# Optimization experiments

Hardware: AMD Instinct MI355X
Metric: run time of the kernel (lower is better)

Reference implementation:

```python
import jax, jax.numpy as jnp
import numpy as np

N_NODES = 1_000_000
N_EDGES = 2_000_000
N_GRAPHS = 50_000
X_DIM = 5
E_DIM = 1
HIDDEN = 110  # num_kernel1_Nhop+..+num_kernel4_Nhop = 10+20+30+50
G_DIM = 5    # graph_embedding_dim
BN_EPS = 1e-5


def setup_inputs() -> dict:
    key = jax.random.key(0)
    ks = jax.random.split(key, 12)
    inp = {
        "x": jax.random.normal(ks[0], (N_NODES, X_DIM), jnp.float32),
        "edge_attr": jax.random.normal(ks[1], (N_EDGES, E_DIM), jnp.float32),
        "batch": jnp.sort(jax.random.randint(ks[2], (N_NODES,), 0, N_GRAPHS)),
        "edge_index": jax.random.randint(ks[3], (2, N_EDGES), 0, N_NODES),
        # BatchNorm affine params
        "bn_x_gamma": jnp.ones((X_DIM,), jnp.float32),
        "bn_x_beta": jnp.zeros((X_DIM,), jnp.float32),
        "bn_e_gamma": jnp.ones((E_DIM,), jnp.float32),
        "bn_e_beta": jnp.zeros((E_DIM,), jnp.float32),
        # stand-in MolGCN params (node transform + edge message mix)
        "W_gnn": jax.random.normal(ks[4], (X_DIM, HIDDEN), jnp.float32) / np.sqrt(X_DIM),
        "b_gnn": jnp.zeros((HIDDEN,), jnp.float32),
        "W_e": jax.random.normal(ks[5], (E_DIM, HIDDEN), jnp.float32),
        # readout head: graph_embedding_lin1 / lin2
        "W1": jax.random.normal(ks[6], (HIDDEN, G_DIM), jnp.float32) / np.sqrt(HIDDEN),
        "b1": jnp.zeros((G_DIM,), jnp.float32),
        "W2": jax.random.normal(ks[7], (G_DIM, G_DIM), jnp.float32) / np.sqrt(G_DIM),
        "b2": jnp.zeros((G_DIM,), jnp.float32),
    }
    return inp


def _batch_norm(v, gamma, beta):
    # train-mode BatchNorm1d math: biased batch statistics
    mu = v.mean(axis=0)
    var = ((v - mu) ** 2).mean(axis=0)
    return (v - mu) * jax.lax.rsqrt(var + BN_EPS) * gamma + beta


def reference(x, edge_attr, batch, edge_index,
              bn_x_gamma, bn_x_beta, bn_e_gamma, bn_e_beta,
              W_gnn, b_gnn, W_e, W1, b1, W2, b2):
    # node / edge batch norms
    xb = _batch_norm(x, bn_x_gamma, bn_x_beta)            # [N, 5]
    eb = _batch_norm(edge_attr, bn_e_gamma, bn_e_beta)    # [E, 1]
    # stand-in MolGCN: linear node transform + scatter-added edge messages
    h = xb @ W_gnn + b_gnn                                # [N, 110]
    msg = jax.ops.segment_sum(eb, edge_index[1], num_segments=x.shape[0])  # [N, 1]
    h = h + msg @ W_e                                     # [N, 110]
    # readout: lin1 -> swish -> dropout(eval=identity) -> lin2
    r = h @ W1 + b1                                       # [N, 5]
    r = r * jax.nn.sigmoid(r)                             # swish
    r = r @ W2 + b2                                       # [N, 5]
    # global_add_pool over graph index
    return jax.ops.segment_sum(r, batch, num_segments=N_GRAPHS)  # [G, 5]
```

## Files before the change

### kernel.cpp

```cpp
#include <hip/hip_runtime.h>
#include <math.h>

#define BN_EPS 1e-5f


__global__ void stats_kernel(const float* __restrict__ x, int N,
                             const float* __restrict__ ea, int E,
                             float* __restrict__ stats) {
    float s[5] = {0, 0, 0, 0, 0};
    float q[5] = {0, 0, 0, 0, 0};
    float es = 0, eq = 0;
    int tid = blockIdx.x * blockDim.x + threadIdx.x;
    int stride = gridDim.x * blockDim.x;

    int nchunks = (int)((5LL * N) / 20);
    for (int c = tid; c < nchunks; c += stride) {
        const float4* p = (const float4*)(x + 20LL * c);
        float4 a0 = p[0], a1 = p[1], a2 = p[2], a3 = p[3], a4 = p[4];
        s[0] += a0.x + a1.y + a2.z + a3.w;
        q[0] += a0.x * a0.x + a1.y * a1.y + a2.z * a2.z + a3.w * a3.w;
        s[1] += a0.y + a1.z + a2.w + a4.x;
        q[1] += a0.y * a0.y + a1.z * a1.z + a2.w * a2.w + a4.x * a4.x;
        s[2] += a0.z + a1.w + a3.x + a4.y;
        q[2] += a0.z * a0.z + a1.w * a1.w + a3.x * a3.x + a4.y * a4.y;
        s[3] += a0.w + a2.x + a3.y + a4.z;
        q[3] += a0.w * a0.w + a2.x * a2.x + a3.y * a3.y + a4.z * a4.z;
        s[4] += a1.x + a2.y + a3.z + a4.w;
        q[4] += a1.x * a1.x + a2.y * a2.y + a3.z * a3.z + a4.w * a4.w;
    }
    for (int n = nchunks * 4 + tid; n < N; n += stride) {
#pragma unroll
        for (int j = 0; j < 5; ++j) {
            float v = x[n * 5 + j];
            s[j] += v;
            q[j] += v * v;
        }
    }
    int evec = E >> 2;
    for (int c = tid; c < evec; c += stride) {
        float4 v = ((const float4*)ea)[c];
        es += v.x + v.y + v.z + v.w;
        eq += v.x * v.x + v.y * v.y + v.z * v.z + v.w * v.w;
    }
    for (int e = (evec << 2) + tid; e < E; e += stride) {
        float v = ea[e];
        es += v;
        eq += v * v;
    }

    float vals[12] = {s[0], s[1], s[2], s[3], s[4], q[0], q[1], q[2], q[3], q[4], es, eq};
#pragma unroll
    for (int j = 0; j < 12; ++j) {
        for (int d = 32; d >= 1; d >>= 1) vals[j] += __shfl_down(vals[j], d);
    }
    __shared__ float bs[4][12];
    int lane = threadIdx.x & 63;
    int wid = threadIdx.x >> 6;
    if (lane == 0) {
#pragma unroll
        for (int j = 0; j < 12; ++j) bs[wid][j] = vals[j];
    }
    __syncthreads();
    if (threadIdx.x < 12) {
        float t = 0;
#pragma unroll
        for (int w = 0; w < 4; ++w) t += bs[w][threadIdx.x];
        atomicAdd(&stats[threadIdx.x], t);
    }
}

__global__ void finalize_kernel(const float* __restrict__ gx, const float* __restrict__ bx,
                                const float* __restrict__ ge, const float* __restrict__ be,
                                const float* __restrict__ Wg, const float* __restrict__ bg,
                                const float* __restrict__ We, const float* __restrict__ W1,
                                const float* __restrict__ b1,
                                const float* __restrict__ stats,
                                float* __restrict__ params, int N, int E) {
    __shared__ float Ms[25], sc[5], sh[5], bg1s[5], we1s[5];
    int t = threadIdx.x;
    if (t < 5) {
        float mu = stats[t] / (float)N;
        float var = stats[5 + t] / (float)N - mu * mu;
        float s = gx[t] * rsqrtf(var + BN_EPS);
        sc[t] = s;
        sh[t] = bx[t] - mu * s;
    }
    if (t < 25) {
        int j = t / 5, i = t % 5;
        float acc = 0;
        for (int k = 0; k < 110; ++k) acc += Wg[j * 110 + k] * W1[k * 5 + i];
        Ms[t] = acc;
    }
    if (t >= 25 && t < 30) {
        int i = t - 25;
        float acc = 0;
        for (int k = 0; k < 110; ++k) acc += We[k] * W1[k * 5 + i];
        we1s[i] = acc;
    }
    if (t >= 30 && t < 35) {
        int i = t - 30;
        float acc = 0;
        for (int k = 0; k < 110; ++k) acc += bg[k] * W1[k * 5 + i];
        bg1s[i] = acc;
    }
    __syncthreads();
    if (t < 25) params[t] = sc[t / 5] * Ms[t];
    if (t < 5) {
        float acc = bg1s[t] + b1[t];
#pragma unroll
        for (int j = 0; j < 5; ++j) acc += sh[j] * Ms[j * 5 + t];
        params[25 + t] = acc;
        params[30 + t] = we1s[t];
    }
    if (t == 35) {
        float mu = stats[10] / (float)E;
        float var = stats[11] / (float)E - mu * mu;
        float s = ge[0] * rsqrtf(var + BN_EPS);
        params[35] = s;
        params[36] = be[0] - mu * s;
    }
}

__global__ void scatter_kernel(const float* __restrict__ ea, const int* __restrict__ dst,
                               int E, const float* __restrict__ params,
                               float* __restrict__ M) {
    float se = params[35];
    float te = params[36];
    int evec = E >> 2;
    int base = blockIdx.x * (blockDim.x * 4) + threadIdx.x;

    float4 v[4];
    int4 d[4];
    bool ok[4];
#pragma unroll
    for (int j = 0; j < 4; ++j) {
        int c = base + j * blockDim.x;
        ok[j] = (c < evec);
        if (ok[j]) {
            v[j] = ((const float4*)ea)[c];
            d[j] = ((const int4*)dst)[c];
        }
    }
#pragma unroll
    for (int j = 0; j < 4; ++j) {
        if (ok[j]) {
            atomicAdd(&M[d[j].x], se * v[j].x + te);
            atomicAdd(&M[d[j].y], se * v[j].y + te);
            atomicAdd(&M[d[j].z], se * v[j].z + te);
            atomicAdd(&M[d[j].w], se * v[j].w + te);
        }
    }
    int gtid = blockIdx.x * blockDim.x + threadIdx.x;
    int gstride = gridDim.x * blockDim.x;
    for (int e = (evec << 2) + gtid; e < E; e += gstride) {
        atomicAdd(&M[dst[e]], se * ea[e] + te);
    }
}

__global__ void node_kernel(const float* __restrict__ x, const int* __restrict__ batch,
                            const float* __restrict__ M,
                            const float* __restrict__ params,
                            const float* __restrict__ W2, const float* __restrict__ b2,
                            float* __restrict__ out, int N) {
    __shared__ float P[37], W2s[25], b2s[5];
    __shared__ float xs[1280];
    int tid = threadIdx.x;
    if (tid < 37) P[tid] = params[tid];
    if (tid < 25) W2s[tid] = W2[tid];
    if (tid < 5) b2s[tid] = b2[tid];

    long long base = (long long)blockIdx.x * 1280;
    int nfl = (int)(5LL * N - base);
    if (nfl > 1280) nfl = 1280;
    const float4* xp = (const float4*)(x + base);
    int nvec = nfl >> 2;
    for (int i = tid; i < nvec; i += 256) ((float4*)xs)[i] = xp[i];
    for (int i = (nvec << 2) + tid; i < nfl; i += 256) xs[i] = x[base + i];
    __syncthreads();

    int n = blockIdx.x * blockDim.x + tid;
    int lane = tid & 63;
    int b = -1;
    float o[5] = {0, 0, 0, 0, 0};
    if (n < N) {
        b = batch[n];
        float msg = M[n];
        float r[5];
#pragma unroll
        for (int i = 0; i < 5; ++i) r[i] = P[25 + i] + msg * P[30 + i];
#pragma unroll
        for (int j = 0; j < 5; ++j) {
            float xv = xs[tid * 5 + j];
#pragma unroll
            for (int i = 0; i < 5; ++i) r[i] += xv * P[j * 5 + i];
        }
#pragma unroll
        for (int i = 0; i < 5; ++i) {
            float v = r[i];
            r[i] = v / (1.0f + __expf(-v));
        }
#pragma unroll
        for (int i = 0; i < 5; ++i) {
            float acc = b2s[i];
#pragma unroll
            for (int k = 0; k < 5; ++k) acc += r[k] * W2s[k * 5 + i];
            o[i] = acc;
        }
    }

#pragma unroll
    for (int d = 1; d < 64; d <<= 1) {
        int nb = __shfl_down(b, d);
        float t0 = __shfl_down(o[0], d);
        float t1 = __shfl_down(o[1], d);
        float t2 = __shfl_down(o[2], d);
        float t3 = __shfl_down(o[3], d);
        float t4 = __shfl_down(o[4], d);
        if (lane + d < 64 && nb == b) {
            o[0] += t0; o[1] += t1; o[2] += t2; o[3] += t3; o[4] += t4;
        }
    }
    int pb = __shfl_up(b, 1);
    bool head = (lane == 0) || (pb != b);
    if (head && b >= 0) {
#pragma unroll
        for (int i = 0; i < 5; ++i) atomicAdd(&out[b * 5 + i], o[i]);
    }
}

extern "C" void kernel_launch(void* const* d_in, const int* in_sizes, int n_in,
                              void* d_out, int out_size, void* d_ws, size_t ws_size,
                              hipStream_t stream) {
    const float* x = (const float*)d_in[0];
    const float* ea = (const float*)d_in[1];
    const int* batch = (const int*)d_in[2];
    const int* ei = (const int*)d_in[3];
    const float* gx = (const float*)d_in[4];
    const float* bx = (const float*)d_in[5];
    const float* ge = (const float*)d_in[6];
    const float* be = (const float*)d_in[7];
    const float* Wg = (const float*)d_in[8];
    const float* bg = (const float*)d_in[9];
    const float* We = (const float*)d_in[10];
    const float* W1 = (const float*)d_in[11];
    const float* b1 = (const float*)d_in[12];
    const float* W2 = (const float*)d_in[13];
    const float* b2 = (const float*)d_in[14];

    int N = in_sizes[2];
    int E = in_sizes[1];

    float* ws = (float*)d_ws;
    float* M = ws;
    float* stats = ws + N;
    float* params = stats + 16;
    float* out = (float*)d_out;

    hipMemsetAsync(d_ws, 0, ((size_t)N + 64) * sizeof(float), stream);
    hipMemsetAsync(d_out, 0, (size_t)out_size * sizeof(float), stream);

    stats_kernel<<<2048, 256, 0, stream>>>(x, N, ea, E, stats);
    finalize_kernel<<<1, 64, 0, stream>>>(gx, bx, ge, be, Wg, bg, We, W1, b1,
                                          stats, params, N, E);

    int evec = E >> 2;
    int sblocks = (evec + 1023) / 1024;
    if (sblocks < 1) sblocks = 1;
    scatter_kernel<<<sblocks, 256, 0, stream>>>(ea, ei + E, E, params, M);

    node_kernel<<<(N + 255) / 256, 256, 0, stream>>>(x, batch, M, params, W2, b2, out, N);
}
```

Measured before the change: 261.7 us.

## Privatize edge scatter per XCC with fixed-point workgroup-scope int atomics

The edge-message scatter now accumulates into eight per-XCC replicas of the node buffer, choosing the replica from the hardware XCC id. It uses relaxed integer atomics on fixed-point values scaled by 2^20 at workgroup scope, so the updates can resolve in the XCC-local L2 instead of device-coherent memory. The node kernel sums the eight replicas and converts back to float. This trades cheaper atomics for eight times the memset and read traffic on the message buffer, adds quantization error, and relies on cross-CU workgroup-scope atomics behaving coherently within an XCC.

```diff
diff --git a/kernel.cpp b/kernel.cpp
--- a/kernel.cpp
+++ b/kernel.cpp
@@ -2,6 +2,8 @@
 #include <math.h>
 
 #define BN_EPS 1e-5f
+#define FXSCALE 1048576.0f
+#define FXINV   (1.0f / 1048576.0f)
 
 
 __global__ void stats_kernel(const float* __restrict__ x, int N,
@@ -123,9 +125,17 @@
 
 __global__ void scatter_kernel(const float* __restrict__ ea, const int* __restrict__ dst,
                                int E, const float* __restrict__ params,
-                               float* __restrict__ M) {
+                               int* __restrict__ Mrep, int N, int R) {
     float se = params[35];
     float te = params[36];
+    int rep = 0;
+    if (R == 8) {
+        unsigned xcc;
+        asm volatile("s_getreg_b32 %0, hwreg(HW_REG_XCC_ID)" : "=s"(xcc));
+        rep = (int)(xcc & 7u);
+    }
+    int* __restrict__ M = Mrep + (size_t)rep * N;
+
     int evec = E >> 2;
     int base = blockIdx.x * (blockDim.x * 4) + threadIdx.x;
 
@@ -141,24 +151,48 @@
             d[j] = ((const int4*)dst)[c];
         }
     }
-#pragma unroll
-    for (int j = 0; j < 4; ++j) {
-        if (ok[j]) {
-            atomicAdd(&M[d[j].x], se * v[j].x + te);
-            atomicAdd(&M[d[j].y], se * v[j].y + te);
-            atomicAdd(&M[d[j].z], se * v[j].z + te);
-            atomicAdd(&M[d[j].w], se * v[j].w + te);
+    if (R == 8) {
+#pragma unroll
+        for (int j = 0; j < 4; ++j) {
+            if (ok[j]) {
+                __hip_atomic_fetch_add(&M[d[j].x], __float2int_rn((se * v[j].x + te) * FXSCALE),
+                                       __ATOMIC_RELAXED, __HIP_MEMORY_SCOPE_WORKGROUP);
+                __hip_atomic_fetch_add(&M[d[j].y], __float2int_rn((se * v[j].y + te) * FXSCALE),
+                                       __ATOMIC_RELAXED, __HIP_MEMORY_SCOPE_WORKGROUP);
+                __hip_atomic_fetch_add(&M[d[j].z], __float2int_rn((se * v[j].z + te) * FXSCALE),
+                                       __ATOMIC_RELAXED, __HIP_MEMORY_SCOPE_WORKGROUP);
+                __hip_atomic_fetch_add(&M[d[j].w], __float2int_rn((se * v[j].w + te) * FXSCALE),
+                                       __ATOMIC_RELAXED, __HIP_MEMORY_SCOPE_WORKGROUP);
+            }
+        }
+    } else {
+#pragma unroll
+        for (int j = 0; j < 4; ++j) {
+            if (ok[j]) {
+                __hip_atomic_fetch_add(&M[d[j].x], __float2int_rn((se * v[j].x + te) * FXSCALE),
+                                       __ATOMIC_RELAXED, __HIP_MEMORY_SCOPE_AGENT);
+                __hip_atomic_fetch_add(&M[d[j].y], __float2int_rn((se * v[j].y + te) * FXSCALE),
+                                       __ATOMIC_RELAXED, __HIP_MEMORY_SCOPE_AGENT);
+                __hip_atomic_fetch_add(&M[d[j].z], __float2int_rn((se * v[j].z + te) * FXSCALE),
+                                       __ATOMIC_RELAXED, __HIP_MEMORY_SCOPE_AGENT);
+                __hip_atomic_fetch_add(&M[d[j].w], __float2int_rn((se * v[j].w + te) * FXSCALE),
+                                       __ATOMIC_RELAXED, __HIP_MEMORY_SCOPE_AGENT);
+            }
         }
     }
     int gtid = blockIdx.x * blockDim.x + threadIdx.x;
     int gstride = gridDim.x * blockDim.x;
     for (int e = (evec << 2) + gtid; e < E; e += gstride) {
-        atomicAdd(&M[dst[e]], se * ea[e] + te);
+        int val = __float2int_rn((se * ea[e] + te) * FXSCALE);
+        if (R == 8)
+            __hip_atomic_fetch_add(&M[dst[e]], val, __ATOMIC_RELAXED, __HIP_MEMORY_SCOPE_WORKGROUP);
+        else
+            __hip_atomic_fetch_add(&M[dst[e]], val, __ATOMIC_RELAXED, __HIP_MEMORY_SCOPE_AGENT);
     }
 }
 
 __global__ void node_kernel(const float* __restrict__ x, const int* __restrict__ batch,
-                            const float* __restrict__ M,
+                            const int* __restrict__ Mrep, int R,
                             const float* __restrict__ params,
                             const float* __restrict__ W2, const float* __restrict__ b2,
                             float* __restrict__ out, int N) {
@@ -184,7 +218,12 @@
     float o[5] = {0, 0, 0, 0, 0};
     if (n < N) {
         b = batch[n];
-        float msg = M[n];
+        int acc = Mrep[n];
+        if (R == 8) {
+#pragma unroll
+            for (int r = 1; r < 8; ++r) acc += Mrep[(size_t)r * N + n];
+        }
+        float msg = (float)acc * FXINV;
         float r[5];
 #pragma unroll
         for (int i = 0; i < 5; ++i) r[i] = P[25 + i] + msg * P[30 + i];
@@ -201,10 +240,10 @@
         }
 #pragma unroll
         for (int i = 0; i < 5; ++i) {
-            float acc = b2s[i];
-#pragma unroll
-            for (int k = 0; k < 5; ++k) acc += r[k] * W2s[k * 5 + i];
-            o[i] = acc;
+            float acc2 = b2s[i];
+#pragma unroll
+            for (int k = 0; k < 5; ++k) acc2 += r[k] * W2s[k * 5 + i];
+            o[i] = acc2;
         }
     }
 
@@ -250,13 +289,15 @@
     int N = in_sizes[2];
     int E = in_sizes[1];
 
-    float* ws = (float*)d_ws;
-    float* M = ws;
-    float* stats = ws + N;
+    size_t needRep = ((size_t)8 * N + 64) * 4;
+    int R = (ws_size >= needRep) ? 8 : 1;
+
+    int* Mrep = (int*)d_ws;
+    float* stats = (float*)d_ws + (size_t)R * N;
     float* params = stats + 16;
     float* out = (float*)d_out;
 
-    hipMemsetAsync(d_ws, 0, ((size_t)N + 64) * sizeof(float), stream);
+    hipMemsetAsync(d_ws, 0, ((size_t)R * N + 64) * sizeof(int), stream);
     hipMemsetAsync(d_out, 0, (size_t)out_size * sizeof(float), stream);
 
     stats_kernel<<<2048, 256, 0, stream>>>(x, N, ea, E, stats);
@@ -266,7 +307,7 @@
     int evec = E >> 2;
     int sblocks = (evec + 1023) / 1024;
     if (sblocks < 1) sblocks = 1;
-    scatter_kernel<<<sblocks, 256, 0, stream>>>(ea, ei + E, E, params, M);
-
-    node_kernel<<<(N + 255) / 256, 256, 0, stream>>>(x, batch, M, params, W2, b2, out, N);
-}
+    scatter_kernel<<<sblocks, 256, 0, stream>>>(ea, ei + E, E, params, Mrep, N, R);
+
+    node_kernel<<<(N + 255) / 256, 256, 0, stream>>>(x, batch, Mrep, R, params, W2, b2, out, N);
+}
```

Result: faster. 246.2 us (-5.9%).
